# Kernel tuning notes

Hardware: AMD Instinct MI355X
Metric: run time of the kernel (lower is better)

Reference implementation:

```python
import jax, jax.numpy as jnp
import numpy as np
import math

B, N, D, O, H = 8, 1024, 512, 512, 8
HD = O // H  # head_dim = 64


def setup_inputs() -> dict:
    key = jax.random.key(0)
    ks = jax.random.split(key, 12)
    x = jax.random.normal(ks[0], (B, N, D), dtype=jnp.float32)
    adj = jax.random.uniform(ks[1], (B, N, N), dtype=jnp.float32)  # unused by forward math
    mask = jax.random.randint(ks[2], (B, N), 0, 2) > 0  # bool padding mask
    # learned params (torch nn.Linear: y = x @ W.T + b)
    qkv_w = jax.random.normal(ks[3], (3 * O, D), dtype=jnp.float32) / math.sqrt(D)
    qkv_b = jnp.zeros((3 * O,), dtype=jnp.float32)
    # self_loop_W: 1/head_dim + U(0,1), per head, non-trainable
    self_loop_W = (1.0 / HD + jax.random.uniform(ks[4], (1, H, 1, 1))).astype(jnp.float32)
    w1 = jax.random.normal(ks[5], (O, O), dtype=jnp.float32) / math.sqrt(O)
    b1 = jnp.zeros((O,), dtype=jnp.float32)
    w2 = jax.random.normal(ks[6], (O, O), dtype=jnp.float32) / math.sqrt(O)
    b2 = jnp.zeros((O,), dtype=jnp.float32)
    wr = jax.random.normal(ks[7], (O, D), dtype=jnp.float32) / math.sqrt(D)
    br = jnp.zeros((O,), dtype=jnp.float32)
    return {"x": x, "adj": adj, "mask": mask, "self_loop_W": self_loop_W,
            "qkv_w": qkv_w, "qkv_b": qkv_b, "w1": w1, "b1": b1,
            "w2": w2, "b2": b2, "wr": wr, "br": br}


def reference(x, adj, mask, self_loop_W, qkv_w, qkv_b, w1, b1, w2, b2, wr, br):
    fmask = mask.astype(x.dtype)  # [B,N]
    # --- MoireAttention ---
    qkv = x @ qkv_w.T + qkv_b                       # [B,N,3O]
    qkv = qkv.reshape(B, N, 3, H, HD).transpose(2, 0, 3, 1, 4)  # [3,B,H,N,hd]
    Q, K, V = qkv[0], qkv[1], qkv[2]
    scores = jnp.einsum('bhnd,bhmd->bhnm', Q, K) / math.sqrt(HD)  # [B,H,N,N]
    eye = jnp.eye(N, dtype=scores.dtype)
    scores = scores + eye[None, None] * self_loop_W  # per-head diagonal self-loop bias
    mask2d = mask[:, None, :, None] & mask[:, None, None, :]  # [B,1,N,N]
    scores = jnp.where(mask2d, scores, jnp.asarray(-1e6, scores.dtype))
    attn = jax.nn.softmax(scores, axis=-1)
    h = jnp.einsum('bhnm,bhmd->bhnd', attn, V)      # [B,H,N,hd]
    h = h.transpose(0, 2, 1, 3).reshape(B, N, O)
    # --- mask, FFN (eval mode: noise/dropout are identity), mask ---
    h = h * fmask[..., None]
    h = jax.nn.relu(h @ w1.T + b1) @ w2.T + b2
    h = h * fmask[..., None]
    # --- residual blend ---
    x_proj = x @ wr.T + br
    return h * 0.5 + x_proj * 0.5
```

## Files before the change

kernel.cpp:

```cpp
#include <hip/hip_runtime.h>
#include <hip/hip_bf16.h>

typedef __attribute__((ext_vector_type(8))) short short8;
typedef __attribute__((ext_vector_type(4))) float f32x4;
typedef __attribute__((ext_vector_type(4))) short short4v;

#define BB 8
#define NN 1024
#define DD 512
#define OO 512
#define HH 8
#define HD 64
#define MM (BB * NN)

#define QSC 0.18033688f
#define KSHIFT -11.54156032f
#define KMASKED -30000.0f

__device__ __forceinline__ void gload_lds16(const void* g, void* l) {
  __builtin_amdgcn_global_load_lds(
      (const __attribute__((address_space(1))) void*)g,
      (__attribute__((address_space(3))) void*)l, 16, 0, 0);
}

__device__ __forceinline__ uint2 cvt4(float4 v) {
  union { uint2 u; __hip_bfloat16 h[4]; } t;
  t.h[0] = __float2bfloat16(v.x);
  t.h[1] = __float2bfloat16(v.y);
  t.h[2] = __float2bfloat16(v.z);
  t.h[3] = __float2bfloat16(v.w);
  return t.u;
}

#define SEG_N 10
struct ConvArgs {
  const float* src[SEG_N];
  __hip_bfloat16* dst[SEG_N];
  int n4[SEG_N];
};

__global__ void convert_kernel(ConvArgs a) {
  const int t = blockIdx.y;
  const int n4 = a.n4[t];
  const float4* fs = (const float4*)a.src[t];
  uint2* d = (uint2*)a.dst[t];
  for (int i = blockIdx.x * blockDim.x + threadIdx.x; i < n4;
       i += gridDim.x * blockDim.x)
    d[i] = cvt4(fs[i]);
}

__global__ __launch_bounds__(256) void gemm_qkv(
    const __hip_bfloat16* __restrict__ A0, const __hip_bfloat16* __restrict__ B0,
    const __hip_bfloat16* __restrict__ bias0, const __hip_bfloat16* __restrict__ bias1,
    __hip_bfloat16* __restrict__ out0, __hip_bfloat16* __restrict__ out1,
    __hip_bfloat16* __restrict__ out2, float* __restrict__ outf, int Kd) {
  __shared__ __align__(16) __hip_bfloat16 smem[16384];

  const int tid  = threadIdx.x;
  const int wave = tid >> 6;
  const int lane = tid & 63;
  const int fl   = lane & 15;
  const int fk   = (lane >> 4) * 8;
  const int wm   = (wave & 1) * 64;
  const int wn   = (wave >> 1) * 64;
  const int bid     = blockIdx.x;
  const int rowpart = 8 * (bid & 7) + ((bid >> 3) & 7);
  const int colpart = bid >> 6;
  const int m0 = rowpart * 128;
  const int n0 = colpart * 128;
  const int glr  = lane >> 2;
  const int glc  = (lane & 3) * 8;

  f32x4 acc[4][4];
#pragma unroll
  for (int i = 0; i < 4; ++i)
#pragma unroll
    for (int j = 0; j < 4; ++j) acc[i][j] = (f32x4){0.f, 0.f, 0.f, 0.f};

  char* lb = (char*)smem;
  for (int k0 = 0; k0 < Kd; k0 += 64) {
    __syncthreads();
    gload_lds16(A0 + (size_t)(m0 + wave * 16 + glr) * Kd + k0 + glc,
                lb + wave * 1024 + lane * 16);
    gload_lds16(A0 + (size_t)(m0 + 64 + wave * 16 + glr) * Kd + k0 + glc,
                lb + (wave + 4) * 1024 + lane * 16);
    gload_lds16(A0 + (size_t)(m0 + wave * 16 + glr) * Kd + k0 + 32 + glc,
                lb + 8192 + wave * 1024 + lane * 16);
    gload_lds16(A0 + (size_t)(m0 + 64 + wave * 16 + glr) * Kd + k0 + 32 + glc,
                lb + 8192 + (wave + 4) * 1024 + lane * 16);
    gload_lds16(B0 + (size_t)(n0 + wave * 16 + glr) * Kd + k0 + glc,
                lb + 16384 + wave * 1024 + lane * 16);
    gload_lds16(B0 + (size_t)(n0 + 64 + wave * 16 + glr) * Kd + k0 + glc,
                lb + 16384 + (wave + 4) * 1024 + lane * 16);
    gload_lds16(B0 + (size_t)(n0 + wave * 16 + glr) * Kd + k0 + 32 + glc,
                lb + 24576 + wave * 1024 + lane * 16);
    gload_lds16(B0 + (size_t)(n0 + 64 + wave * 16 + glr) * Kd + k0 + 32 + glc,
                lb + 24576 + (wave + 4) * 1024 + lane * 16);
    __syncthreads();

#pragma unroll
    for (int kh = 0; kh < 2; ++kh) {
      const __hip_bfloat16* Ap = smem + kh * 4096;
      const __hip_bfloat16* Bp = smem + 8192 + kh * 4096;
      short8 af[4], bfr[4];
#pragma unroll
      for (int i = 0; i < 4; ++i)
        af[i] = *(const short8*)&Ap[(wm + i * 16 + fl) * 32 + fk];
#pragma unroll
      for (int j = 0; j < 4; ++j)
        bfr[j] = *(const short8*)&Bp[(wn + j * 16 + fl) * 32 + fk];
#pragma unroll
      for (int i = 0; i < 4; ++i)
#pragma unroll
        for (int j = 0; j < 4; ++j)
          acc[i][j] = __builtin_amdgcn_mfma_f32_16x16x32_bf16(af[i], bfr[j],
                                                              acc[i][j], 0, 0, 0);
    }
  }

  const int rb = (lane >> 4) * 4;
  const int part = n0 >> 9;
  if (part < 2) {
    __hip_bfloat16* dst = (part == 0) ? out0 : out1;
    const float scf = (part == 0) ? QSC : 1.0f;
#pragma unroll
    for (int j = 0; j < 4; ++j) {
      const int colb  = n0 + wn + j * 16;
      const int o     = colb & 511;
      const int headq = o >> 6;
      const int d     = (o & 63) + fl;
      const float bi  = __bfloat162float(bias0[colb + fl]);
#pragma unroll
      for (int i = 0; i < 4; ++i) {
#pragma unroll
        for (int r = 0; r < 4; ++r) {
          const int row = m0 + wm + i * 16 + rb + r;
          const int bb  = row >> 10;
          const int nn  = row & 1023;
          dst[((size_t)((bb << 3) + headq) * NN + nn) * HD + d] =
              __float2bfloat16((acc[i][j][r] + bi) * scf);
        }
      }
    }
  } else if (part == 2) {
    __syncthreads();
    __hip_bfloat16* tsc = smem + wave * 1120;
    const int bb  = (m0 + wm) >> 10;
    const int nnb = (m0 + wm) & 1023;
    const int dl  = lane >> 2;
    const int cc  = (lane & 3) * 16;
#pragma unroll
    for (int j = 0; j < 4; ++j) {
      const int colb  = n0 + wn + j * 16;
      const int o     = colb & 511;
      const int headq = o >> 6;
      const int dbase = o & 63;
      const float bi  = __bfloat162float(bias0[colb + fl]);
#pragma unroll
      for (int i = 0; i < 4; ++i) {
#pragma unroll
        for (int r = 0; r < 4; ++r) {
          const int rr = i * 16 + rb + r;
          tsc[fl * 70 + rr] = __float2bfloat16(acc[i][j][r] + bi);
        }
      }
      uint4 r0 = *(const uint4*)&tsc[dl * 70 + cc];
      uint4 r1 = *(const uint4*)&tsc[dl * 70 + cc + 8];
      __hip_bfloat16* vdst =
          out2 + ((size_t)((bb << 3) + headq) * HD + dbase + dl) * NN + nnb;
      *(uint4*)&vdst[cc] = r0;
      *(uint4*)&vdst[cc + 8] = r1;
    }
  } else {
#pragma unroll
    for (int j = 0; j < 4; ++j) {
      const int colb = n0 + wn + j * 16;
      const int o    = colb & 511;
      const float bi = 0.5f * __bfloat162float(bias1[o + fl]);
#pragma unroll
      for (int i = 0; i < 4; ++i) {
#pragma unroll
        for (int r = 0; r < 4; ++r) {
          const int row = m0 + wm + i * 16 + rb + r;
          outf[(size_t)row * OO + o + fl] = 0.5f * acc[i][j][r] + bi;
        }
      }
    }
  }
}

__global__ __launch_bounds__(1024) void ffn_fused(
    const __hip_bfloat16* __restrict__ hb,
    const __hip_bfloat16* __restrict__ w1, const __hip_bfloat16* __restrict__ w2,
    const __hip_bfloat16* __restrict__ b1, const __hip_bfloat16* __restrict__ b2,
    const int* __restrict__ mask, float* __restrict__ outf) {
  __shared__ __align__(16) __hip_bfloat16 h1s[32 * 520];
  __shared__ float Mrow[32];

  const int tid  = threadIdx.x;
  const int wv   = tid >> 6;
  const int lane = tid & 63;
  const int fl   = lane & 15;
  const int quad = lane >> 4;
  const int fk   = quad * 8;
  const int m0   = blockIdx.x * 32;

  {
    const int col = (tid & 63) * 8;
#pragma unroll
    for (int c = 0; c < 2; ++c) {
      const int row = c * 16 + (tid >> 6);
      *(uint4*)&h1s[row * 520 + col] =
          *(const uint4*)&hb[(size_t)(m0 + row) * OO + col];
    }
    if (tid < 32) Mrow[tid] = (mask[m0 + tid] != 0) ? 1.f : 0.f;
  }
  __syncthreads();

  f32x4 acc[2][2];

  auto run_phase = [&](const __hip_bfloat16* __restrict__ W) {
    const __hip_bfloat16* wl0 = W + (size_t)(wv * 32 + fl) * 512 + fk;
    short8 a[6][2];
#pragma unroll
    for (int d = 0; d < 6; ++d)
#pragma unroll
      for (int j = 0; j < 2; ++j)
        a[d][j] = *(const short8*)(wl0 + d * 32 + j * 8192);
#pragma unroll
    for (int k = 0; k < 16; ++k) {
      short8 bh_[2];
#pragma unroll
      for (int i = 0; i < 2; ++i)
        bh_[i] = *(const short8*)&h1s[(i * 16 + fl) * 520 + k * 32 + fk];
      __builtin_amdgcn_s_setprio(1);
#pragma unroll
      for (int j = 0; j < 2; ++j)
#pragma unroll
        for (int i = 0; i < 2; ++i)
          acc[i][j] = __builtin_amdgcn_mfma_f32_16x16x32_bf16(a[k % 6][j], bh_[i],
                                                              acc[i][j], 0, 0, 0);
      __builtin_amdgcn_s_setprio(0);
      if (k < 10) {
#pragma unroll
        for (int j = 0; j < 2; ++j)
          a[k % 6][j] = *(const short8*)(wl0 + (k + 6) * 32 + j * 8192);
      }
      __builtin_amdgcn_sched_barrier(0);
    }
  };

#pragma unroll
  for (int i = 0; i < 2; ++i)
#pragma unroll
    for (int j = 0; j < 2; ++j) acc[i][j] = (f32x4){0.f, 0.f, 0.f, 0.f};
  run_phase(w1);
  __syncthreads();

#pragma unroll
  for (int j = 0; j < 2; ++j) {
    const int c0 = wv * 32 + j * 16 + quad * 4;
    union { short4v s; __hip_bfloat16 h[4]; } bv;
    bv.s = *(const short4v*)&b1[c0];
#pragma unroll
    for (int i = 0; i < 2; ++i) {
      const float mr = Mrow[i * 16 + fl];
      union { short4v s; __hip_bfloat16 h[4]; } pu;
#pragma unroll
      for (int e = 0; e < 4; ++e) {
        const float v = fmaxf(acc[i][j][e] + __bfloat162float(bv.h[e]), 0.f) * mr;
        pu.h[e] = __float2bfloat16(v);
      }
      *(short4v*)&h1s[(i * 16 + fl) * 520 + c0] = pu.s;
    }
  }
  __syncthreads();

#pragma unroll
  for (int i = 0; i < 2; ++i)
#pragma unroll
    for (int j = 0; j < 2; ++j) acc[i][j] = (f32x4){0.f, 0.f, 0.f, 0.f};
  run_phase(w2);

#pragma unroll
  for (int j = 0; j < 2; ++j) {
    const int c0 = wv * 32 + j * 16 + quad * 4;
    union { short4v s; __hip_bfloat16 h[4]; } b2v;
    b2v.s = *(const short4v*)&b2[c0];
#pragma unroll
    for (int i = 0; i < 2; ++i) {
      const float mr = Mrow[i * 16 + fl];
      const int row = m0 + i * 16 + fl;
      float4 prev = *(const float4*)&outf[(size_t)row * OO + c0];
      float4 o;
      o.x = prev.x + 0.5f * (acc[i][j][0] + mr * __bfloat162float(b2v.h[0]));
      o.y = prev.y + 0.5f * (acc[i][j][1] + mr * __bfloat162float(b2v.h[1]));
      o.z = prev.z + 0.5f * (acc[i][j][2] + mr * __bfloat162float(b2v.h[2]));
      o.w = prev.w + 0.5f * (acc[i][j][3] + mr * __bfloat162float(b2v.h[3]));
      *(float4*)&outf[(size_t)row * OO + c0] = o;
    }
  }
}

__global__ __launch_bounds__(256) void attn_kernel(
    const __hip_bfloat16* __restrict__ Qb, const __hip_bfloat16* __restrict__ Kb,
    const __hip_bfloat16* __restrict__ Vt, const __hip_bfloat16* __restrict__ slw,
    const int* __restrict__ mask, __hip_bfloat16* __restrict__ hb) {
  __shared__ __align__(16) __hip_bfloat16 QPs[128 * 72];
  __shared__ __align__(16) __hip_bfloat16 Ks[2][64 * 72];
  __shared__ __align__(16) __hip_bfloat16 Vs[2][64 * 72];
  __shared__ float Msf[NN];

  const int tid  = threadIdx.x;
  const int wave = tid >> 6;
  const int lane = tid & 63;
  const int fl   = lane & 15;
  const int quad = lane >> 4;
  const int fk   = quad * 8;
  const int rb   = quad * 4;
  const int bh   = blockIdx.x & 63;
  const int qblk = blockIdx.x >> 6;
  const int b    = bh >> 3;
  const int head = bh & 7;
  const int q0   = qblk * 128;

  const float slwL2 = __bfloat162float(slw[head]) * 1.44269504f;

  const int r16A = 8 * qblk + 2 * wave;
  const int r16B = r16A + 1;
  const int kbdA = r16A >> 2, jdA = r16A & 3;
  const int kbdB = r16B >> 2, jdB = r16B & 3;

  const int srow2 = tid >> 2;
  const int sc2   = (tid & 3) * 16;
  const __hip_bfloat16* kgb = Kb + (size_t)bh * NN * HD;
  const __hip_bfloat16* vgb = Vt + (size_t)bh * HD * NN;

  uint4 kr0 = *(const uint4*)(kgb + (size_t)srow2 * HD + sc2);
  uint4 kr1 = *(const uint4*)(kgb + (size_t)srow2 * HD + sc2 + 8);
  uint4 vr0 = *(const uint4*)(vgb + (size_t)srow2 * NN + sc2);
  uint4 vr1 = *(const uint4*)(vgb + (size_t)srow2 * NN + sc2 + 8);
  {
    const int qr = tid >> 1;
    const int qc = (tid & 1) * 32;
    const __hip_bfloat16* qg = Qb + ((size_t)bh * NN + q0 + qr) * HD + qc;
    uint4 v0 = *(const uint4*)(qg);
    uint4 v1 = *(const uint4*)(qg + 8);
    uint4 v2 = *(const uint4*)(qg + 16);
    uint4 v3 = *(const uint4*)(qg + 24);
    *(uint4*)&QPs[qr * 72 + qc] = v0;
    *(uint4*)&QPs[qr * 72 + qc + 8] = v1;
    *(uint4*)&QPs[qr * 72 + qc + 16] = v2;
    *(uint4*)&QPs[qr * 72 + qc + 24] = v3;
#pragma unroll
    for (int k = 0; k < 4; ++k) {
      const int idx = tid * 4 + k;
      Msf[idx] = (mask[b * NN + idx] != 0) ? KSHIFT : KMASKED;
    }
  }
  *(uint4*)&Ks[0][srow2 * 72 + sc2] = kr0;
  *(uint4*)&Ks[0][srow2 * 72 + sc2 + 8] = kr1;
  *(uint4*)&Vs[0][srow2 * 72 + sc2] = vr0;
  *(uint4*)&Vs[0][srow2 * 72 + sc2 + 8] = vr1;
  kr0 = *(const uint4*)(kgb + (size_t)(64 + srow2) * HD + sc2);
  kr1 = *(const uint4*)(kgb + (size_t)(64 + srow2) * HD + sc2 + 8);
  vr0 = *(const uint4*)(vgb + (size_t)srow2 * NN + 64 + sc2);
  vr1 = *(const uint4*)(vgb + (size_t)srow2 * NN + 64 + sc2 + 8);
  __syncthreads();
  const short8 qa0A = *(const short8*)&QPs[(wave * 32 + fl) * 72 + fk];
  const short8 qa1A = *(const short8*)&QPs[(wave * 32 + fl) * 72 + fk + 32];
  const short8 qa0B = *(const short8*)&QPs[(wave * 32 + 16 + fl) * 72 + fk];
  const short8 qa1B = *(const short8*)&QPs[(wave * 32 + 16 + fl) * 72 + fk + 32];

  float lsumA = 0.f, lsumB = 0.f;
  f32x4 OaccA[4], OaccB[4];
#pragma unroll
  for (int t = 0; t < 4; ++t) {
    OaccA[t] = (f32x4){0.f, 0.f, 0.f, 0.f};
    OaccB[t] = (f32x4){0.f, 0.f, 0.f, 0.f};
  }

  for (int kb = 0; kb < NN / 64; ++kb) {
    const int kbase = kb * 64;
    const int cur   = kb & 1;
    const __hip_bfloat16* Kc = Ks[cur];
    const __hip_bfloat16* Vc = Vs[cur];

    f32x4 sfrA[4], sfrB[4];
    __builtin_amdgcn_s_setprio(1);
#pragma unroll
    for (int j = 0; j < 4; ++j) {
      const short8 kf0 = *(const short8*)&Kc[(j * 16 + fl) * 72 + fk];
      const short8 kf1 = *(const short8*)&Kc[(j * 16 + fl) * 72 + fk + 32];
      f32x4 zA = (f32x4){0.f, 0.f, 0.f, 0.f};
      zA = __builtin_amdgcn_mfma_f32_16x16x32_bf16(kf0, qa0A, zA, 0, 0, 0);
      zA = __builtin_amdgcn_mfma_f32_16x16x32_bf16(kf1, qa1A, zA, 0, 0, 0);
      sfrA[j] = zA;
      f32x4 zB = (f32x4){0.f, 0.f, 0.f, 0.f};
      zB = __builtin_amdgcn_mfma_f32_16x16x32_bf16(kf0, qa0B, zB, 0, 0, 0);
      zB = __builtin_amdgcn_mfma_f32_16x16x32_bf16(kf1, qa1B, zB, 0, 0, 0);
      sfrB[j] = zB;
    }
    __builtin_amdgcn_s_setprio(0);

    if ((fl >> 2) == quad && (kb == kbdA || kb == kbdB)) {
#pragma unroll
      for (int j = 0; j < 4; ++j)
#pragma unroll
        for (int e = 0; e < 4; ++e)
          if ((fl & 3) == e) {
            if (kb == kbdA && j == jdA) sfrA[j][e] += slwL2;
            if (kb == kbdB && j == jdB) sfrB[j][e] += slwL2;
          }
    }

#pragma unroll
    for (int j = 0; j < 4; ++j) {
      const f32x4 mb4 = *(const f32x4*)&Msf[kbase + j * 16 + quad * 4];
      union { short4v s; __hip_bfloat16 h[4]; } puA, puB;
      float psA = 0.f, psB = 0.f;
#pragma unroll
      for (int e = 0; e < 4; ++e) {
        const float pvA = exp2f(sfrA[j][e] + mb4[e]);
        psA += pvA;
        puA.h[e] = __float2bfloat16(pvA);
        const float pvB = exp2f(sfrB[j][e] + mb4[e]);
        psB += pvB;
        puB.h[e] = __float2bfloat16(pvB);
      }
      lsumA += psA;
      lsumB += psB;
      *(short4v*)&QPs[(wave * 32 + fl) * 72 + j * 16 + quad * 4] = puA.s;
      *(short4v*)&QPs[(wave * 32 + 16 + fl) * 72 + j * 16 + quad * 4] = puB.s;
    }

    const short8 paA0 = *(const short8*)&QPs[(wave * 32 + fl) * 72 + fk];
    const short8 paA1 = *(const short8*)&QPs[(wave * 32 + fl) * 72 + fk + 32];
    const short8 paB0 = *(const short8*)&QPs[(wave * 32 + 16 + fl) * 72 + fk];
    const short8 paB1 = *(const short8*)&QPs[(wave * 32 + 16 + fl) * 72 + fk + 32];
    __builtin_amdgcn_s_setprio(1);
#pragma unroll
    for (int t = 0; t < 4; ++t) {
      const short8 vf0 = *(const short8*)&Vc[(t * 16 + fl) * 72 + fk];
      const short8 vf1 = *(const short8*)&Vc[(t * 16 + fl) * 72 + fk + 32];
      OaccA[t] = __builtin_amdgcn_mfma_f32_16x16x32_bf16(paA0, vf0, OaccA[t], 0, 0, 0);
      OaccA[t] = __builtin_amdgcn_mfma_f32_16x16x32_bf16(paA1, vf1, OaccA[t], 0, 0, 0);
      OaccB[t] = __builtin_amdgcn_mfma_f32_16x16x32_bf16(paB0, vf0, OaccB[t], 0, 0, 0);
      OaccB[t] = __builtin_amdgcn_mfma_f32_16x16x32_bf16(paB1, vf1, OaccB[t], 0, 0, 0);
    }
    __builtin_amdgcn_s_setprio(0);

    if (kb + 1 < NN / 64) {
      *(uint4*)&Ks[cur ^ 1][srow2 * 72 + sc2] = kr0;
      *(uint4*)&Ks[cur ^ 1][srow2 * 72 + sc2 + 8] = kr1;
      *(uint4*)&Vs[cur ^ 1][srow2 * 72 + sc2] = vr0;
      *(uint4*)&Vs[cur ^ 1][srow2 * 72 + sc2 + 8] = vr1;
      if (kb + 2 < NN / 64) {
        const int nk = kbase + 128;
        kr0 = *(const uint4*)(kgb + (size_t)(nk + srow2) * HD + sc2);
        kr1 = *(const uint4*)(kgb + (size_t)(nk + srow2) * HD + sc2 + 8);
        vr0 = *(const uint4*)(vgb + (size_t)srow2 * NN + nk + sc2);
        vr1 = *(const uint4*)(vgb + (size_t)srow2 * NN + nk + sc2 + 8);
      }
      __builtin_amdgcn_sched_barrier(0);
      __syncthreads();
    }
  }

#pragma unroll
  for (int f = 0; f < 2; ++f) {
    float l = (f == 0) ? lsumA : lsumB;
    l += __shfl_xor(l, 16, 64);
    l += __shfl_xor(l, 32, 64);
    const int qrow_me = q0 + wave * 32 + f * 16 + fl;
    const float qm = (mask[b * NN + qrow_me] != 0) ? 1.f : 0.f;
    const float sf = qm / fmaxf(l, 1e-30f);
    float scl[4];
#pragma unroll
    for (int r = 0; r < 4; ++r) scl[r] = __shfl(sf, rb + r, 64);
#pragma unroll
    for (int t = 0; t < 4; ++t) {
      const int d = t * 16 + fl;
#pragma unroll
      for (int r = 0; r < 4; ++r) {
        const int qrow_g = q0 + wave * 32 + f * 16 + rb + r;
        const float ov = (f == 0) ? OaccA[t][r] : OaccB[t][r];
        hb[(size_t)(b * NN + qrow_g) * OO + head * HD + d] =
            __float2bfloat16(ov * scl[r]);
      }
    }
  }
}

extern "C" void kernel_launch(void* const* d_in, const int* in_sizes, int n_in,
                              void* d_out, int out_size, void* d_ws, size_t ws_size,
                              hipStream_t stream) {
  const float* x_raw    = (const float*)d_in[0];
  const int* mask       = (const int*)d_in[2];
  const float* slw_raw  = (const float*)d_in[3];
  const float* qkvw_raw = (const float*)d_in[4];
  const float* qkvb_raw = (const float*)d_in[5];
  const float* w1_raw   = (const float*)d_in[6];
  const float* b1_raw   = (const float*)d_in[7];
  const float* w2_raw   = (const float*)d_in[8];
  const float* b2_raw   = (const float*)d_in[9];
  const float* wr_raw   = (const float*)d_in[10];
  const float* br_raw   = (const float*)d_in[11];
  float* outf           = (float*)d_out;

  __hip_bfloat16* p = (__hip_bfloat16*)d_ws;
  __hip_bfloat16* xc    = p; p += (size_t)MM * DD;
  __hip_bfloat16* qkvwc = p; p += 3 * OO * DD;
  __hip_bfloat16* wrc   = p; p += OO * DD;
  __hip_bfloat16* w1c   = p; p += OO * OO;
  __hip_bfloat16* w2c   = p; p += OO * OO;
  __hip_bfloat16* qkvbc = p; p += 3 * OO;
  __hip_bfloat16* b1c   = p; p += OO;
  __hip_bfloat16* b2c   = p; p += OO;
  __hip_bfloat16* brc   = p; p += OO;
  __hip_bfloat16* slwc  = p; p += 64;
  const size_t ebuf = (size_t)BB * HH * NN * HD;
  __hip_bfloat16* Qb = p; p += ebuf;
  __hip_bfloat16* Kb = p; p += ebuf;
  __hip_bfloat16* Vb = p; p += ebuf;
  __hip_bfloat16* hb = p; p += ebuf;

  if (ws_size < (size_t)((char*)p - (char*)d_ws)) return;

  ConvArgs ca;
  ca.src[0] = x_raw;    ca.dst[0] = xc;    ca.n4[0] = MM * DD / 4;
  ca.src[1] = qkvw_raw; ca.dst[1] = qkvwc; ca.n4[1] = 3 * OO * DD / 4;
  ca.src[2] = w1_raw;   ca.dst[2] = w1c;   ca.n4[2] = OO * OO / 4;
  ca.src[3] = w2_raw;   ca.dst[3] = w2c;   ca.n4[3] = OO * OO / 4;
  ca.src[4] = wr_raw;   ca.dst[4] = wrc;   ca.n4[4] = OO * DD / 4;
  ca.src[5] = qkvb_raw; ca.dst[5] = qkvbc; ca.n4[5] = 3 * OO / 4;
  ca.src[6] = b1_raw;   ca.dst[6] = b1c;   ca.n4[6] = OO / 4;
  ca.src[7] = b2_raw;   ca.dst[7] = b2c;   ca.n4[7] = OO / 4;
  ca.src[8] = br_raw;   ca.dst[8] = brc;   ca.n4[8] = OO / 4;
  ca.src[9] = slw_raw;  ca.dst[9] = slwc;  ca.n4[9] = HH / 4;
  convert_kernel<<<dim3(1024, SEG_N), 256, 0, stream>>>(ca);

  gemm_qkv<<<1024, 256, 0, stream>>>(xc, qkvwc, qkvbc, brc, Qb, Kb, Vb, outf, DD);
  attn_kernel<<<BB * HH * (NN / 128), 256, 0, stream>>>(Qb, Kb, Vb, slwc, mask, hb);
  ffn_fused<<<256, 1024, 0, stream>>>(hb, w1c, w2c, b1c, b2c, mask, outf);
}
```

Baseline: 210.1 us.

## Software-pipeline attention loop: overlap next-tile QK with current PV

Restructures the flash-attention inner loop so each iteration computes QK^T for the next key tile, then P·V for the current tile, then softmax for the next tile. These pieces are independent, so the scheduler can interleave MFMA work with exp and conversion work. K/V LDS buffers grow from double to triple buffering so the next tile can be staged while the current V tile is still being read. The larger LDS footprint may reduce how many blocks fit per CU, and register pressure rises.

Result: no change. 209.7 us (-0.2%).

```diff
diff --git a/kernel.cpp b/kernel.cpp
--- a/kernel.cpp
+++ b/kernel.cpp
@@ -307,8 +307,8 @@
     const __hip_bfloat16* __restrict__ Vt, const __hip_bfloat16* __restrict__ slw,
     const int* __restrict__ mask, __hip_bfloat16* __restrict__ hb) {
   __shared__ __align__(16) __hip_bfloat16 QPs[128 * 72];
-  __shared__ __align__(16) __hip_bfloat16 Ks[2][64 * 72];
-  __shared__ __align__(16) __hip_bfloat16 Vs[2][64 * 72];
+  __shared__ __align__(16) __hip_bfloat16 Ks[3][64 * 72];
+  __shared__ __align__(16) __hip_bfloat16 Vs[3][64 * 72];
   __shared__ float Msf[NN];
 
   const int tid  = threadIdx.x;
@@ -380,13 +380,9 @@
     OaccB[t] = (f32x4){0.f, 0.f, 0.f, 0.f};
   }
 
-  for (int kb = 0; kb < NN / 64; ++kb) {
-    const int kbase = kb * 64;
-    const int cur   = kb & 1;
-    const __hip_bfloat16* Kc = Ks[cur];
-    const __hip_bfloat16* Vc = Vs[cur];
-
-    f32x4 sfrA[4], sfrB[4];
+  f32x4 sfrA[4], sfrB[4];
+
+  auto qk_tile = [&](const __hip_bfloat16* Kc) {
     __builtin_amdgcn_s_setprio(1);
 #pragma unroll
     for (int j = 0; j < 4; ++j) {
@@ -402,18 +398,20 @@
       sfrB[j] = zB;
     }
     __builtin_amdgcn_s_setprio(0);
-
-    if ((fl >> 2) == quad && (kb == kbdA || kb == kbdB)) {
+  };
+
+  auto softmax_tile = [&](int kb2) {
+    if ((fl >> 2) == quad && (kb2 == kbdA || kb2 == kbdB)) {
 #pragma unroll
       for (int j = 0; j < 4; ++j)
 #pragma unroll
         for (int e = 0; e < 4; ++e)
           if ((fl & 3) == e) {
-            if (kb == kbdA && j == jdA) sfrA[j][e] += slwL2;
-            if (kb == kbdB && j == jdB) sfrB[j][e] += slwL2;
+            if (kb2 == kbdA && j == jdA) sfrA[j][e] += slwL2;
+            if (kb2 == kbdB && j == jdB) sfrB[j][e] += slwL2;
           }
     }
-
+    const int kbase = kb2 * 64;
 #pragma unroll
     for (int j = 0; j < 4; ++j) {
       const f32x4 mb4 = *(const f32x4*)&Msf[kbase + j * 16 + quad * 4];
@@ -433,7 +431,9 @@
       *(short4v*)&QPs[(wave * 32 + fl) * 72 + j * 16 + quad * 4] = puA.s;
       *(short4v*)&QPs[(wave * 32 + 16 + fl) * 72 + j * 16 + quad * 4] = puB.s;
     }
-
+  };
+
+  auto pv_tile = [&](const __hip_bfloat16* Vc) {
     const short8 paA0 = *(const short8*)&QPs[(wave * 32 + fl) * 72 + fk];
     const short8 paA1 = *(const short8*)&QPs[(wave * 32 + fl) * 72 + fk + 32];
     const short8 paB0 = *(const short8*)&QPs[(wave * 32 + 16 + fl) * 72 + fk];
@@ -449,23 +449,33 @@
       OaccB[t] = __builtin_amdgcn_mfma_f32_16x16x32_bf16(paB1, vf1, OaccB[t], 0, 0, 0);
     }
     __builtin_amdgcn_s_setprio(0);
-
-    if (kb + 1 < NN / 64) {
-      *(uint4*)&Ks[cur ^ 1][srow2 * 72 + sc2] = kr0;
-      *(uint4*)&Ks[cur ^ 1][srow2 * 72 + sc2 + 8] = kr1;
-      *(uint4*)&Vs[cur ^ 1][srow2 * 72 + sc2] = vr0;
-      *(uint4*)&Vs[cur ^ 1][srow2 * 72 + sc2 + 8] = vr1;
-      if (kb + 2 < NN / 64) {
-        const int nk = kbase + 128;
-        kr0 = *(const uint4*)(kgb + (size_t)(nk + srow2) * HD + sc2);
-        kr1 = *(const uint4*)(kgb + (size_t)(nk + srow2) * HD + sc2 + 8);
-        vr0 = *(const uint4*)(vgb + (size_t)srow2 * NN + nk + sc2);
-        vr1 = *(const uint4*)(vgb + (size_t)srow2 * NN + nk + sc2 + 8);
-      }
-      __builtin_amdgcn_sched_barrier(0);
-      __syncthreads();
-    }
-  }
+  };
+
+  qk_tile(Ks[0]);
+  softmax_tile(0);
+
+  for (int kb = 0; kb < NN / 64 - 1; ++kb) {
+    const int nxt = kb + 1;
+    const int nb  = nxt % 3;
+    *(uint4*)&Ks[nb][srow2 * 72 + sc2] = kr0;
+    *(uint4*)&Ks[nb][srow2 * 72 + sc2 + 8] = kr1;
+    *(uint4*)&Vs[nb][srow2 * 72 + sc2] = vr0;
+    *(uint4*)&Vs[nb][srow2 * 72 + sc2 + 8] = vr1;
+    if (kb + 2 < NN / 64) {
+      const int nk = (kb + 2) * 64;
+      kr0 = *(const uint4*)(kgb + (size_t)(nk + srow2) * HD + sc2);
+      kr1 = *(const uint4*)(kgb + (size_t)(nk + srow2) * HD + sc2 + 8);
+      vr0 = *(const uint4*)(vgb + (size_t)srow2 * NN + nk + sc2);
+      vr1 = *(const uint4*)(vgb + (size_t)srow2 * NN + nk + sc2 + 8);
+    }
+    __builtin_amdgcn_sched_barrier(0);
+    __syncthreads();
+
+    qk_tile(Ks[nb]);
+    pv_tile(Vs[kb % 3]);
+    softmax_tile(nxt);
+  }
+  pv_tile(Vs[(NN / 64 - 1) % 3]);
 
 #pragma unroll
   for (int f = 0; f < 2; ++f) {
```
